# Kernel tuning notes

Measured on AMD Instinct MI355X. Metric: run time of the kernel, lower is better.

Reference implementation:

```python
import jax, jax.numpy as jnp
import numpy as np

THRESHOLD = 0.7  # masking_strategy.confidence_threshold


def setup_inputs() -> dict:
    key = jax.random.key(0)
    ks = jax.random.split(key, 6)
    B, S, V, D = 4, 1024, 50257, 768
    H = D // 2
    logits = jax.random.normal(ks[0], (B, S, V), dtype=jnp.float32)
    hidden_states = jax.random.normal(ks[1], (B, S, D), dtype=jnp.float32)
    current_mask = jax.random.randint(ks[2], (B, S), 0, 2) > 0
    w1 = jax.random.normal(ks[3], (D, H), dtype=jnp.float32) * 0.02
    b1 = jnp.zeros((H,), dtype=jnp.float32)
    w2 = jax.random.normal(ks[4], (H, 1), dtype=jnp.float32) * 0.02
    b2 = jnp.zeros((1,), dtype=jnp.float32)
    return {"logits": logits, "hidden_states": hidden_states,
            "current_mask": current_mask, "w1": w1, "b1": b1, "w2": w2,
            "b2": b2, "step": 8, "total_steps": 8}


def _confidence(logits, hidden_states, current_mask, w1, b1, w2, b2):
    # Fast-dLLM confidence: 0.8 * max softmax prob + 0.2 * learned head, zeroed off-mask
    lse = jax.scipy.special.logsumexp(logits, axis=-1)          # [B,S]
    max_prob = jnp.exp(jnp.max(logits, axis=-1) - lse)          # [B,S]
    h = jax.nn.gelu(hidden_states @ w1 + b1, approximate=False)  # [B,S,D//2]
    learned = jax.nn.sigmoid((h @ w2 + b2).squeeze(-1))          # [B,S]
    conf = 0.8 * max_prob + 0.2 * learned
    return conf * current_mask.astype(conf.dtype)


def reference(logits, hidden_states, current_mask, w1, b1, w2, b2, step, total_steps):
    B, S, V = logits.shape
    conf = _confidence(logits, hidden_states, current_mask, w1, b1, w2, b2)

    masked_conf = jnp.where(current_mask, conf, -jnp.inf)        # [B,S]
    above = current_mask & (conf > THRESHOLD)                    # [B,S]
    any_above = jnp.any(above, axis=1, keepdims=True)            # [B,1]
    has_masked = jnp.any(current_mask, axis=1, keepdims=True)    # [B,1]

    # fallback: unmask the single highest-confidence masked position
    best = jnp.argmax(masked_conf, axis=1)                       # [B]
    fallback = (jnp.arange(S)[None, :] == best[:, None]) & has_masked

    unmask = jnp.where(any_above, above, fallback) & has_masked  # [B,S]
    new_mask = current_mask & ~unmask

    if step < total_steps // 2:
        # multinomial sampling == argmax over logits + Gumbel noise
        g = -jnp.log(-jnp.log(jax.random.uniform(jax.random.key(42), logits.shape,
                                                 minval=1e-20, maxval=1.0)))
        tokens = jnp.argmax(logits + g, axis=-1)
    else:
        tokens = jnp.argmax(logits, axis=-1)                     # [B,S]

    unmasked_tokens = jnp.where(unmask, tokens, 0).astype(jnp.int32)
    return conf, new_mask, unmasked_tokens
```

## Files before the change

### kernel.cpp

```cpp
#include <hip/hip_runtime.h>
#include <float.h>
#include <stdint.h>
#include <math.h>

#define B_ 4
#define S_ 1024
#define V_ 50257
#define D_ 768
#define H_ 384
#define BS_ (B_ * S_)

__global__ __launch_bounds__(256) void k_logits_stats(
    const float* __restrict__ logits, float* __restrict__ maxprob,
    int* __restrict__ amax) {
  const int row = blockIdx.x;
  const int tid = threadIdx.x;
  const float* __restrict__ p = logits + (size_t)row * V_;

  const int lead = (int)(((16u - (unsigned)((uintptr_t)p & 15u)) & 15u) >> 2);
  const int nvec = (V_ - lead) >> 2;
  const int tail = V_ - lead - (nvec << 2);

  float m = -FLT_MAX;
  int idx = 0;
  float s0 = 0.f, s1 = 0.f, s2 = 0.f, s3 = 0.f;

  if (tid < lead) {
    float x = p[tid];
    s0 += __expf(x);
    m = x; idx = tid;
  }
  const float4* __restrict__ pv = (const float4*)(p + lead);
  for (int j = tid; j < nvec; j += 256) {
    float4 x = pv[j];
    int base = lead + (j << 2);
    s0 += __expf(x.x); if (x.x > m) { m = x.x; idx = base;     }
    s1 += __expf(x.y); if (x.y > m) { m = x.y; idx = base + 1; }
    s2 += __expf(x.z); if (x.z > m) { m = x.z; idx = base + 2; }
    s3 += __expf(x.w); if (x.w > m) { m = x.w; idx = base + 3; }
  }
  if (tid < tail) {
    int i = lead + (nvec << 2) + tid;
    float x = p[i];
    s0 += __expf(x);
    if (x > m) { m = x; idx = i; }
  }
  float s = (s0 + s1) + (s2 + s3);

  for (int off = 32; off > 0; off >>= 1) {
    float om = __shfl_down(m, off);
    int   oi = __shfl_down(idx, off);
    float os = __shfl_down(s, off);
    s += os;
    if (om > m || (om == m && oi < idx)) { m = om; idx = oi; }
  }
  __shared__ float wm[4], wsv[4];
  __shared__ int wiv[4];
  const int lane = tid & 63, wave = tid >> 6;
  if (lane == 0) { wm[wave] = m; wiv[wave] = idx; wsv[wave] = s; }
  __syncthreads();
  if (tid == 0) {
    for (int k = 1; k < 4; k++) {
      s += wsv[k];
      if (wm[k] > m || (wm[k] == m && wiv[k] < idx)) { m = wm[k]; idx = wiv[k]; }
    }
    maxprob[row] = __expf(m) / s;
    amax[row] = idx;
  }
}

__global__ __launch_bounds__(384) void k_mlp(
    const float* __restrict__ hidden, const float* __restrict__ w1,
    const float* __restrict__ b1, const float* __restrict__ w2,
    const float* __restrict__ b2, float* __restrict__ learned) {
  __shared__ float h_lds[16 * D_];
  __shared__ float red[16];
  const int tid = threadIdx.x;
  const int pos0 = blockIdx.x * 16;

  if (tid < 16) red[tid] = 0.f;

  const float4* __restrict__ src = (const float4*)(hidden + (size_t)pos0 * D_);
  float4* dst = (float4*)h_lds;
  for (int i = tid; i < 16 * D_ / 4; i += 384) dst[i] = src[i];
  __syncthreads();

  const int jg = tid % 96;
  const int pg = tid / 96;
  const int j0 = jg * 4;
  const int p0 = pg * 4;

  float acc[4][4];
#pragma unroll
  for (int a = 0; a < 4; a++)
#pragma unroll
    for (int b = 0; b < 4; b++) acc[a][b] = 0.f;

  for (int d = 0; d < D_; d += 4) {
    float w[4][4];
#pragma unroll
    for (int dd = 0; dd < 4; dd++) {
      float4 t = *(const float4*)(w1 + (size_t)(d + dd) * H_ + j0);
      w[dd][0] = t.x; w[dd][1] = t.y; w[dd][2] = t.z; w[dd][3] = t.w;
    }
#pragma unroll
    for (int pp = 0; pp < 4; pp++) {
      float4 t = *(const float4*)(&h_lds[(p0 + pp) * D_ + d]);
      float h0 = t.x, h1 = t.y, h2 = t.z, h3 = t.w;
#pragma unroll
      for (int jj = 0; jj < 4; jj++)
        acc[pp][jj] += h0 * w[0][jj] + h1 * w[1][jj] + h2 * w[2][jj] + h3 * w[3][jj];
    }
  }

  float4 b1v = *(const float4*)(b1 + j0);
  float4 w2v = *(const float4*)(w2 + j0);
  float b1a[4] = {b1v.x, b1v.y, b1v.z, b1v.w};
  float w2a[4] = {w2v.x, w2v.y, w2v.z, w2v.w};
#pragma unroll
  for (int pp = 0; pp < 4; pp++) {
    float part = 0.f;
#pragma unroll
    for (int jj = 0; jj < 4; jj++) {
      float z = acc[pp][jj] + b1a[jj];
      float g = 0.5f * z * (1.0f + erff(z * 0.70710678118654752f));
      part += g * w2a[jj];
    }
    atomicAdd(&red[p0 + pp], part);
  }
  __syncthreads();
  if (tid < 16) {
    float z = red[tid] + b2[0];
    learned[pos0 + tid] = 1.0f / (1.0f + expf(-z));
  }
}

__global__ __launch_bounds__(1024) void k_finalize(
    const float* __restrict__ maxprob, const int* __restrict__ amax,
    const float* __restrict__ learned, const int* __restrict__ mask,
    float* __restrict__ out) {
  const int b = blockIdx.x;
  const int s = threadIdx.x;
  const int row = b * S_ + s;

  const bool msk = mask[row] != 0;
  const float conf = 0.8f * maxprob[row] + 0.2f * learned[row];
  const bool above = msk && (conf > 0.7f);
  const float mc = msk ? conf : -FLT_MAX;

  __shared__ int s_any, s_has, s_best;
  __shared__ float wv[16];
  __shared__ int wi[16];
  if (s == 0) { s_any = 0; s_has = 0; }
  __syncthreads();

  unsigned long long ba = __ballot(above);
  unsigned long long bm = __ballot(msk);
  const int lane = s & 63, wave = s >> 6;
  if (lane == 0) {
    if (ba) atomicOr(&s_any, 1);
    if (bm) atomicOr(&s_has, 1);
  }

  float v = mc; int i = s;
  for (int off = 32; off > 0; off >>= 1) {
    float ov = __shfl_down(v, off);
    int   oi = __shfl_down(i, off);
    if (ov > v || (ov == v && oi < i)) { v = ov; i = oi; }
  }
  if (lane == 0) { wv[wave] = v; wi[wave] = i; }
  __syncthreads();
  if (s == 0) {
    float bv = wv[0]; int bi = wi[0];
    for (int k = 1; k < 16; k++)
      if (wv[k] > bv || (wv[k] == bv && wi[k] < bi)) { bv = wv[k]; bi = wi[k]; }
    s_best = bi;
  }
  __syncthreads();

  const bool any_above = s_any != 0;
  const bool has = s_has != 0;
  const bool unmask = any_above ? above : (has && (s == s_best));
  const bool nm = msk && !unmask;

  out[row] = msk ? conf : 0.0f;
  out[BS_ + row] = nm ? 1.0f : 0.0f;
  out[2 * BS_ + row] = (float)(unmask ? amax[row] : 0);
}

extern "C" void kernel_launch(void* const* d_in, const int* in_sizes, int n_in,
                              void* d_out, int out_size, void* d_ws, size_t ws_size,
                              hipStream_t stream) {
  const float* logits = (const float*)d_in[0];
  const float* hidden = (const float*)d_in[1];
  const int* mask = (const int*)d_in[2];
  const float* w1 = (const float*)d_in[3];
  const float* b1 = (const float*)d_in[4];
  const float* w2 = (const float*)d_in[5];
  const float* b2 = (const float*)d_in[6];
  float* out = (float*)d_out;

  float* ws = (float*)d_ws;
  float* maxprob = ws;
  int* amax = (int*)(ws + BS_);
  float* learned = ws + 2 * BS_;

  k_logits_stats<<<BS_, 256, 0, stream>>>(logits, maxprob, amax);
  k_mlp<<<BS_ / 16, 384, 0, stream>>>(hidden, w1, b1, w2, b2, learned);
  k_finalize<<<B_, S_, 0, stream>>>(maxprob, amax, learned, mask, out);
}
```

Before: 1.151 ms.

## Fuse logits-stats and MLP kernels into one heterogeneous launch with unrolled loads

Merges the logits reduction kernel and the confidence-head MLP kernel into a single launch. The first blocks run the MLP and the rest run per-row logits stats, so the compute-heavy MLP can overlap with the memory-bound logits scan and one launch boundary goes away. The logits path now uses 384 threads with a 3-way unrolled float4 load loop to keep more loads in flight. The trade-off is that every block reserves the MLP's ~48KB LDS, which limits occupancy for the logits blocks, and the launch_bounds occupancy hint may increase register pressure.

```diff
diff --git a/kernel.cpp b/kernel.cpp
--- a/kernel.cpp
+++ b/kernel.cpp
@@ -9,129 +9,155 @@
 #define D_ 768
 #define H_ 384
 #define BS_ (B_ * S_)
-
-__global__ __launch_bounds__(256) void k_logits_stats(
-    const float* __restrict__ logits, float* __restrict__ maxprob,
-    int* __restrict__ amax) {
-  const int row = blockIdx.x;
+#define MLPB_ (BS_ / 16)
+#define FT_ 384
+
+__global__ __launch_bounds__(FT_, 5) void k_fused(
+    const float* __restrict__ logits, const float* __restrict__ hidden,
+    const float* __restrict__ w1, const float* __restrict__ b1,
+    const float* __restrict__ w2, const float* __restrict__ b2,
+    float* __restrict__ maxprob, int* __restrict__ amax,
+    float* __restrict__ learned) {
+  __shared__ float lds[16 * D_ + 16];
   const int tid = threadIdx.x;
-  const float* __restrict__ p = logits + (size_t)row * V_;
-
-  const int lead = (int)(((16u - (unsigned)((uintptr_t)p & 15u)) & 15u) >> 2);
-  const int nvec = (V_ - lead) >> 2;
-  const int tail = V_ - lead - (nvec << 2);
-
-  float m = -FLT_MAX;
-  int idx = 0;
-  float s0 = 0.f, s1 = 0.f, s2 = 0.f, s3 = 0.f;
-
-  if (tid < lead) {
-    float x = p[tid];
-    s0 += __expf(x);
-    m = x; idx = tid;
-  }
-  const float4* __restrict__ pv = (const float4*)(p + lead);
-  for (int j = tid; j < nvec; j += 256) {
-    float4 x = pv[j];
-    int base = lead + (j << 2);
-    s0 += __expf(x.x); if (x.x > m) { m = x.x; idx = base;     }
-    s1 += __expf(x.y); if (x.y > m) { m = x.y; idx = base + 1; }
-    s2 += __expf(x.z); if (x.z > m) { m = x.z; idx = base + 2; }
-    s3 += __expf(x.w); if (x.w > m) { m = x.w; idx = base + 3; }
-  }
-  if (tid < tail) {
-    int i = lead + (nvec << 2) + tid;
-    float x = p[i];
-    s0 += __expf(x);
-    if (x > m) { m = x; idx = i; }
-  }
-  float s = (s0 + s1) + (s2 + s3);
-
-  for (int off = 32; off > 0; off >>= 1) {
-    float om = __shfl_down(m, off);
-    int   oi = __shfl_down(idx, off);
-    float os = __shfl_down(s, off);
-    s += os;
-    if (om > m || (om == m && oi < idx)) { m = om; idx = oi; }
-  }
-  __shared__ float wm[4], wsv[4];
-  __shared__ int wiv[4];
-  const int lane = tid & 63, wave = tid >> 6;
-  if (lane == 0) { wm[wave] = m; wiv[wave] = idx; wsv[wave] = s; }
-  __syncthreads();
-  if (tid == 0) {
-    for (int k = 1; k < 4; k++) {
-      s += wsv[k];
-      if (wm[k] > m || (wm[k] == m && wiv[k] < idx)) { m = wm[k]; idx = wiv[k]; }
-    }
-    maxprob[row] = __expf(m) / s;
-    amax[row] = idx;
-  }
-}
-
-__global__ __launch_bounds__(384) void k_mlp(
-    const float* __restrict__ hidden, const float* __restrict__ w1,
-    const float* __restrict__ b1, const float* __restrict__ w2,
-    const float* __restrict__ b2, float* __restrict__ learned) {
-  __shared__ float h_lds[16 * D_];
-  __shared__ float red[16];
-  const int tid = threadIdx.x;
-  const int pos0 = blockIdx.x * 16;
-
-  if (tid < 16) red[tid] = 0.f;
-
-  const float4* __restrict__ src = (const float4*)(hidden + (size_t)pos0 * D_);
-  float4* dst = (float4*)h_lds;
-  for (int i = tid; i < 16 * D_ / 4; i += 384) dst[i] = src[i];
-  __syncthreads();
-
-  const int jg = tid % 96;
-  const int pg = tid / 96;
-  const int j0 = jg * 4;
-  const int p0 = pg * 4;
-
-  float acc[4][4];
-#pragma unroll
-  for (int a = 0; a < 4; a++)
-#pragma unroll
-    for (int b = 0; b < 4; b++) acc[a][b] = 0.f;
-
-  for (int d = 0; d < D_; d += 4) {
-    float w[4][4];
-#pragma unroll
-    for (int dd = 0; dd < 4; dd++) {
-      float4 t = *(const float4*)(w1 + (size_t)(d + dd) * H_ + j0);
-      w[dd][0] = t.x; w[dd][1] = t.y; w[dd][2] = t.z; w[dd][3] = t.w;
-    }
+
+  if (blockIdx.x < MLPB_) {
+    float* h_lds = lds;
+    float* red = lds + 16 * D_;
+    const int pos0 = blockIdx.x * 16;
+
+    if (tid < 16) red[tid] = 0.f;
+
+    const float4* __restrict__ src = (const float4*)(hidden + (size_t)pos0 * D_);
+    float4* dst = (float4*)h_lds;
+    for (int i = tid; i < 16 * D_ / 4; i += FT_) dst[i] = src[i];
+    __syncthreads();
+
+    const int jg = tid % 96;
+    const int pg = tid / 96;
+    const int j0 = jg * 4;
+    const int p0 = pg * 4;
+
+    float acc[4][4];
+#pragma unroll
+    for (int a = 0; a < 4; a++)
+#pragma unroll
+      for (int b = 0; b < 4; b++) acc[a][b] = 0.f;
+
+    for (int d = 0; d < D_; d += 4) {
+      float w[4][4];
+#pragma unroll
+      for (int dd = 0; dd < 4; dd++) {
+        float4 t = *(const float4*)(w1 + (size_t)(d + dd) * H_ + j0);
+        w[dd][0] = t.x; w[dd][1] = t.y; w[dd][2] = t.z; w[dd][3] = t.w;
+      }
+#pragma unroll
+      for (int pp = 0; pp < 4; pp++) {
+        float4 t = *(const float4*)(&h_lds[(p0 + pp) * D_ + d]);
+        float h0 = t.x, h1 = t.y, h2 = t.z, h3 = t.w;
+#pragma unroll
+        for (int jj = 0; jj < 4; jj++)
+          acc[pp][jj] += h0 * w[0][jj] + h1 * w[1][jj] + h2 * w[2][jj] + h3 * w[3][jj];
+      }
+    }
+
+    float4 b1v = *(const float4*)(b1 + j0);
+    float4 w2v = *(const float4*)(w2 + j0);
+    float b1a[4] = {b1v.x, b1v.y, b1v.z, b1v.w};
+    float w2a[4] = {w2v.x, w2v.y, w2v.z, w2v.w};
 #pragma unroll
     for (int pp = 0; pp < 4; pp++) {
-      float4 t = *(const float4*)(&h_lds[(p0 + pp) * D_ + d]);
-      float h0 = t.x, h1 = t.y, h2 = t.z, h3 = t.w;
-#pragma unroll
-      for (int jj = 0; jj < 4; jj++)
-        acc[pp][jj] += h0 * w[0][jj] + h1 * w[1][jj] + h2 * w[2][jj] + h3 * w[3][jj];
-    }
-  }
-
-  float4 b1v = *(const float4*)(b1 + j0);
-  float4 w2v = *(const float4*)(w2 + j0);
-  float b1a[4] = {b1v.x, b1v.y, b1v.z, b1v.w};
-  float w2a[4] = {w2v.x, w2v.y, w2v.z, w2v.w};
-#pragma unroll
-  for (int pp = 0; pp < 4; pp++) {
-    float part = 0.f;
-#pragma unroll
-    for (int jj = 0; jj < 4; jj++) {
-      float z = acc[pp][jj] + b1a[jj];
-      float g = 0.5f * z * (1.0f + erff(z * 0.70710678118654752f));
-      part += g * w2a[jj];
-    }
-    atomicAdd(&red[p0 + pp], part);
-  }
-  __syncthreads();
-  if (tid < 16) {
-    float z = red[tid] + b2[0];
-    learned[pos0 + tid] = 1.0f / (1.0f + expf(-z));
+      float part = 0.f;
+#pragma unroll
+      for (int jj = 0; jj < 4; jj++) {
+        float z = acc[pp][jj] + b1a[jj];
+        float g = 0.5f * z * (1.0f + erff(z * 0.70710678118654752f));
+        part += g * w2a[jj];
+      }
+      atomicAdd(&red[p0 + pp], part);
+    }
+    __syncthreads();
+    if (tid < 16) {
+      float z = red[tid] + b2[0];
+      learned[pos0 + tid] = 1.0f / (1.0f + expf(-z));
+    }
+  } else {
+    const int row = blockIdx.x - MLPB_;
+    const float* __restrict__ p = logits + (size_t)row * V_;
+
+    const int lead = (int)(((16u - (unsigned)((uintptr_t)p & 15u)) & 15u) >> 2);
+    const int nvec = (V_ - lead) >> 2;
+    const int tail = V_ - lead - (nvec << 2);
+
+    float m = -FLT_MAX;
+    int idx = 0;
+    float s0 = 0.f, s1 = 0.f, s2 = 0.f, s3 = 0.f;
+
+    if (tid < lead) {
+      float x = p[tid];
+      s0 += __expf(x);
+      m = x; idx = tid;
+    }
+    const float4* __restrict__ pv = (const float4*)(p + lead);
+
+    int j = tid;
+    for (; j + 2 * FT_ < nvec; j += 3 * FT_) {
+      float4 x0 = pv[j];
+      float4 x1 = pv[j + FT_];
+      float4 x2 = pv[j + 2 * FT_];
+      int b0 = lead + (j << 2);
+      s0 += __expf(x0.x); if (x0.x > m) { m = x0.x; idx = b0;     }
+      s1 += __expf(x0.y); if (x0.y > m) { m = x0.y; idx = b0 + 1; }
+      s2 += __expf(x0.z); if (x0.z > m) { m = x0.z; idx = b0 + 2; }
+      s3 += __expf(x0.w); if (x0.w > m) { m = x0.w; idx = b0 + 3; }
+      int b1i = b0 + (FT_ << 2);
+      s0 += __expf(x1.x); if (x1.x > m) { m = x1.x; idx = b1i;     }
+      s1 += __expf(x1.y); if (x1.y > m) { m = x1.y; idx = b1i + 1; }
+      s2 += __expf(x1.z); if (x1.z > m) { m = x1.z; idx = b1i + 2; }
+      s3 += __expf(x1.w); if (x1.w > m) { m = x1.w; idx = b1i + 3; }
+      int b2i = b1i + (FT_ << 2);
+      s0 += __expf(x2.x); if (x2.x > m) { m = x2.x; idx = b2i;     }
+      s1 += __expf(x2.y); if (x2.y > m) { m = x2.y; idx = b2i + 1; }
+      s2 += __expf(x2.z); if (x2.z > m) { m = x2.z; idx = b2i + 2; }
+      s3 += __expf(x2.w); if (x2.w > m) { m = x2.w; idx = b2i + 3; }
+    }
+    for (; j < nvec; j += FT_) {
+      float4 x = pv[j];
+      int base = lead + (j << 2);
+      s0 += __expf(x.x); if (x.x > m) { m = x.x; idx = base;     }
+      s1 += __expf(x.y); if (x.y > m) { m = x.y; idx = base + 1; }
+      s2 += __expf(x.z); if (x.z > m) { m = x.z; idx = base + 2; }
+      s3 += __expf(x.w); if (x.w > m) { m = x.w; idx = base + 3; }
+    }
+    if (tid < tail) {
+      int i = lead + (nvec << 2) + tid;
+      float x = p[i];
+      s0 += __expf(x);
+      if (x > m) { m = x; idx = i; }
+    }
+    float s = (s0 + s1) + (s2 + s3);
+
+    for (int off = 32; off > 0; off >>= 1) {
+      float om = __shfl_down(m, off);
+      int   oi = __shfl_down(idx, off);
+      float os = __shfl_down(s, off);
+      s += os;
+      if (om > m || (om == m && oi < idx)) { m = om; idx = oi; }
+    }
+    float* wm  = lds;
+    float* wsv = lds + 8;
+    int*   wiv = (int*)(lds + 16);
+    const int lane = tid & 63, wave = tid >> 6;
+    if (lane == 0) { wm[wave] = m; wiv[wave] = idx; wsv[wave] = s; }
+    __syncthreads();
+    if (tid == 0) {
+      for (int k = 1; k < 6; k++) {
+        s += wsv[k];
+        if (wm[k] > m || (wm[k] == m && wiv[k] < idx)) { m = wm[k]; idx = wiv[k]; }
+      }
+      maxprob[row] = __expf(m) / s;
+      amax[row] = idx;
+    }
   }
 }
 
@@ -205,7 +231,7 @@
   int* amax = (int*)(ws + BS_);
   float* learned = ws + 2 * BS_;
 
-  k_logits_stats<<<BS_, 256, 0, stream>>>(logits, maxprob, amax);
-  k_mlp<<<BS_ / 16, 384, 0, stream>>>(hidden, w1, b1, w2, b2, learned);
+  k_fused<<<MLPB_ + BS_, FT_, 0, stream>>>(logits, hidden, w1, b1, w2, b2,
+                                           maxprob, amax, learned);
   k_finalize<<<B_, S_, 0, stream>>>(maxprob, amax, learned, mask, out);
 }
```

Result: faster. 1.061 ms (-7.8%).
